# Kernel optimization log

Hardware: AMD Instinct MI355X
Metric: run time of the kernel (lower is better)

## Reference

```python
import jax, jax.numpy as jnp
import numpy as np

STATE_DIM = 16
CHANNELS = 256
LENGTH = 8192
SAMPLE_RATE = 100.0


def setup_inputs() -> dict:
    key = jax.random.key(0)
    ks = jax.random.split(key, 4)
    fan = 1.0 / np.sqrt(CHANNELS)  # lecun-normal-ish scale, flax Dense default
    x = jax.random.normal(ks[0], (LENGTH, CHANNELS), dtype=jnp.float32)
    logA = jnp.log(1.0 + jnp.arange(STATE_DIM, dtype=jnp.float32))  # module's Ainit
    W_dt = jax.random.normal(ks[1], (CHANNELS, CHANNELS), dtype=jnp.float32) * fan
    b_dt = jnp.zeros((CHANNELS,), dtype=jnp.float32)
    W_B = jax.random.normal(ks[2], (CHANNELS, STATE_DIM), dtype=jnp.float32) * fan
    b_B = jnp.zeros((STATE_DIM,), dtype=jnp.float32)
    W_C = jax.random.normal(ks[3], (CHANNELS, STATE_DIM), dtype=jnp.float32) * fan
    b_C = jnp.zeros((STATE_DIM,), dtype=jnp.float32)
    return {"x": x, "logA": logA, "W_dt": W_dt, "b_dt": b_dt,
            "W_B": W_B, "b_B": b_B, "W_C": W_C, "b_C": b_C}


def reference(x, logA, W_dt, b_dt, W_B, b_B, W_C, b_C):
    # x: (L, C)
    A = -jnp.exp(logA)                                   # (S,)
    dt = jax.nn.softplus(1.0 / SAMPLE_RATE + x @ W_dt + b_dt)  # (L, C)
    B = 1.0 + x @ W_B + b_B                              # (L, S)
    C = x @ W_C + b_C                                    # (L, S)
    # discretize: Adiscr = exp(A * dt), shape (L, C, S)
    Adiscr = jnp.exp(dt[:, :, None] * A[None, None, :])
    # Bdiscr = exp((Adiscr - 1) * (B / A))  (faithful to source, incl. outer exp)
    Bdiscr = jnp.exp((Adiscr - 1.0) * (B / A)[:, None, :])  # (L, C, S)
    u = Bdiscr * x[:, :, None]                           # (L, C, S)

    def ssm_scan(p1, p2):
        (A1, c1), (A2, c2) = p1, p2
        return (A2 * A1, c2 + A2 * c1)

    _, h = jax.lax.associative_scan(ssm_scan, (Adiscr, u))  # h: (L, C, S)
    y = jnp.einsum('ls,lcs->lc', C, h)                    # (L, C)
    return y
```

## Files before the change

### kernel.cpp

```cpp
#include <hip/hip_runtime.h>
#include <hip/hip_bf16.h>
#include <math.h>

#define LL 8192
#define CC 256
#define SS 16
#define NJ (CC*SS)
#define GG 512
#define TT 16
#define SEGS 16
#define PER (GG/SEGS)

#define LOG2E 1.4426950408889634f
#define LN2   0.6931471805599453f

typedef __attribute__((ext_vector_type(8))) short short8;
typedef __attribute__((ext_vector_type(4))) float floatx4;

__device__ __forceinline__ float fexp2(float v){ return __builtin_amdgcn_exp2f(v); }
__device__ __forceinline__ float flog2v(float v){ return __builtin_amdgcn_logf(v); }

__device__ __forceinline__ float softplus(float z){
    float t = fexp2(-fabsf(z) * LOG2E);
    return fmaxf(z, 0.f) + LN2 * flog2v(1.f + t);
}

__device__ __forceinline__ void load16(float* d, const float* __restrict__ p){
    *(float4*)&d[0]  = *(const float4*)&p[0];
    *(float4*)&d[4]  = *(const float4*)&p[4];
    *(float4*)&d[8]  = *(const float4*)&p[8];
    *(float4*)&d[12] = *(const float4*)&p[12];
}

__device__ __forceinline__ unsigned short f2b(float f){
    __hip_bfloat16 h = __float2bfloat16(f);
    return *(unsigned short*)&h;
}
__device__ __forceinline__ float b2f(unsigned short u){
    __hip_bfloat16 h = *(__hip_bfloat16*)&u;
    return __bfloat162float(h);
}

#define MBM 64
#define MBN 32
#define MBK 64
#define ASTR 72

__global__ __launch_bounds__(256,4) void k_mm(
    const float* __restrict__ x,
    const float* __restrict__ Wdt, const float* __restrict__ WB,
    const float* __restrict__ WC,
    const float* __restrict__ bdt, const float* __restrict__ bB,
    const float* __restrict__ bC, const float* __restrict__ logA,
    float* __restrict__ dt, float* __restrict__ boa, float* __restrict__ cm)
{
    __shared__ unsigned short Ah[MBM*ASTR];
    __shared__ unsigned short Al[MBM*ASTR];
    __shared__ unsigned short Bh[MBN*ASTR];
    __shared__ unsigned short Bl[MBN*ASTR];

    const int tid  = threadIdx.x;
    const int row0 = blockIdx.x * MBM;
    const int n0   = blockIdx.y * MBN;

    const int lane = tid & 63;
    const int wv   = tid >> 6;
    const int wm   = wv >> 1;
    const int wn   = wv & 1;
    const int m16  = lane & 15;
    const int q    = lane >> 4;

    const int bn  = tid & 31;
    const int bkb = (tid >> 5) * 8;
    const int bcol = n0 + bn;
    const float* __restrict__ wp;
    int wstride;
    if (bcol < 256)      { wp = Wdt + bcol;       wstride = CC; }
    else if (bcol < 272) { wp = WB  + (bcol-256); wstride = SS; }
    else                 { wp = WC  + (bcol-272); wstride = SS; }

    floatx4 acc[2];
    acc[0] = (floatx4){0.f,0.f,0.f,0.f};
    acc[1] = (floatx4){0.f,0.f,0.f,0.f};

    for (int k0 = 0; k0 < CC; k0 += MBK) {
        __syncthreads();
        #pragma unroll
        for (int h2 = 0; h2 < 2; h2++){
            int chunk = tid + h2*256;
            int r    = chunk >> 3;
            int koff = (chunk & 7) * 8;
            float4 f0 = *(const float4*)&x[(size_t)(row0+r)*CC + k0 + koff];
            float4 f1 = *(const float4*)&x[(size_t)(row0+r)*CC + k0 + koff + 4];
            float fv[8] = {f0.x,f0.y,f0.z,f0.w,f1.x,f1.y,f1.z,f1.w};
            unsigned short hs[8], ls[8];
            #pragma unroll
            for (int i=0;i<8;i++){
                hs[i] = f2b(fv[i]);
                ls[i] = f2b(fv[i] - b2f(hs[i]));
            }
            uint4 ph, pl;
            ph.x = (unsigned)hs[0] | ((unsigned)hs[1] << 16);
            ph.y = (unsigned)hs[2] | ((unsigned)hs[3] << 16);
            ph.z = (unsigned)hs[4] | ((unsigned)hs[5] << 16);
            ph.w = (unsigned)hs[6] | ((unsigned)hs[7] << 16);
            pl.x = (unsigned)ls[0] | ((unsigned)ls[1] << 16);
            pl.y = (unsigned)ls[2] | ((unsigned)ls[3] << 16);
            pl.z = (unsigned)ls[4] | ((unsigned)ls[5] << 16);
            pl.w = (unsigned)ls[6] | ((unsigned)ls[7] << 16);
            *(uint4*)&Ah[r*ASTR + koff] = ph;
            *(uint4*)&Al[r*ASTR + koff] = pl;
        }
        {
            unsigned short hs[8], ls[8];
            #pragma unroll
            for (int i=0;i<8;i++){
                float v = wp[(size_t)(k0 + bkb + i)*wstride];
                hs[i] = f2b(v);
                ls[i] = f2b(v - b2f(hs[i]));
            }
            uint4 ph, pl;
            ph.x = (unsigned)hs[0] | ((unsigned)hs[1] << 16);
            ph.y = (unsigned)hs[2] | ((unsigned)hs[3] << 16);
            ph.z = (unsigned)hs[4] | ((unsigned)hs[5] << 16);
            ph.w = (unsigned)hs[6] | ((unsigned)hs[7] << 16);
            pl.x = (unsigned)ls[0] | ((unsigned)ls[1] << 16);
            pl.y = (unsigned)ls[2] | ((unsigned)ls[3] << 16);
            pl.z = (unsigned)ls[4] | ((unsigned)ls[5] << 16);
            pl.w = (unsigned)ls[6] | ((unsigned)ls[7] << 16);
            *(uint4*)&Bh[bn*ASTR + bkb] = ph;
            *(uint4*)&Bl[bn*ASTR + bkb] = pl;
        }
        __syncthreads();

        #pragma unroll
        for (int ks = 0; ks < MBK; ks += 32) {
            short8 bh = *(const short8*)&Bh[(wn*16 + m16)*ASTR + ks + q*8];
            short8 bl = *(const short8*)&Bl[(wn*16 + m16)*ASTR + ks + q*8];
            #pragma unroll
            for (int mt = 0; mt < 2; mt++){
                short8 ah = *(const short8*)&Ah[(wm*32 + mt*16 + m16)*ASTR + ks + q*8];
                short8 al = *(const short8*)&Al[(wm*32 + mt*16 + m16)*ASTR + ks + q*8];
                acc[mt] = __builtin_amdgcn_mfma_f32_16x16x32_bf16(al, bh, acc[mt], 0, 0, 0);
                acc[mt] = __builtin_amdgcn_mfma_f32_16x16x32_bf16(ah, bl, acc[mt], 0, 0, 0);
                acc[mt] = __builtin_amdgcn_mfma_f32_16x16x32_bf16(ah, bh, acc[mt], 0, 0, 0);
            }
        }
    }

    const int col = n0 + wn*16 + m16;
    if (col < 256) {
        float bias = bdt[col];
        #pragma unroll
        for (int mt = 0; mt < 2; mt++){
            #pragma unroll
            for (int r = 0; r < 4; r++){
                int row = row0 + wm*32 + mt*16 + q*4 + r;
                dt[(size_t)row*CC + col] = softplus(0.01f + acc[mt][r] + bias);
            }
        }
    } else if (col < 272) {
        int s = col - 256;
        float A = -fexp2(logA[s] * LOG2E);
        float sc = LOG2E / A;
        float bias = bB[s];
        #pragma unroll
        for (int mt = 0; mt < 2; mt++){
            #pragma unroll
            for (int r = 0; r < 4; r++){
                int row = row0 + wm*32 + mt*16 + q*4 + r;
                boa[(size_t)row*SS + s] = (1.f + acc[mt][r] + bias) * sc;
            }
        }
    } else {
        int s = col - 272;
        float bias = bC[s];
        #pragma unroll
        for (int mt = 0; mt < 2; mt++){
            #pragma unroll
            for (int r = 0; r < 4; r++){
                int row = row0 + wm*32 + mt*16 + q*4 + r;
                cm[(size_t)row*SS + s] = acc[mt][r] + bias;
            }
        }
    }
}

__global__ __launch_bounds__(256) void k_scan1(const float* __restrict__ dt,
    const float* __restrict__ x, const float* __restrict__ boa,
    const float* __restrict__ logA,
    float* __restrict__ Ap, float* __restrict__ Hl)
{
    const int c = threadIdx.x;
    const int g = blockIdx.x;
    const int row0 = g * TT;

    __shared__ float boS[TT*SS];
    boS[c] = boa[(size_t)row0*SS + c];

    float Al2[SS];
    #pragma unroll
    for (int s=0;s<SS;s++) Al2[s] = -fexp2(logA[s]*LOG2E) * LOG2E;

    const float* __restrict__ dp = dt + (size_t)row0*CC + c;
    const float* __restrict__ xp = x  + (size_t)row0*CC + c;

    float Apr[SS], h[SS];
    #pragma unroll
    for (int s=0;s<SS;s++){ Apr[s]=1.f; h[s]=0.f; }

    __syncthreads();

    #pragma unroll
    for (int t=0;t<TT;t++){
        float d  = dp[t*CC];
        float xv = xp[t*CC];
        float bo[SS]; load16(bo, &boS[t*SS]);
        #pragma unroll
        for (int s=0;s<SS;s++){
            float a = fexp2(d * Al2[s]);
            float u = fexp2(fmaf(a, bo[s], -bo[s])) * xv;
            h[s] = fmaf(a, h[s], u);
            Apr[s] *= a;
        }
    }

    const size_t base = (size_t)g*NJ + c*SS;
    *(float4*)&Ap[base+0]  = make_float4(Apr[0],Apr[1],Apr[2],Apr[3]);
    *(float4*)&Ap[base+4]  = make_float4(Apr[4],Apr[5],Apr[6],Apr[7]);
    *(float4*)&Ap[base+8]  = make_float4(Apr[8],Apr[9],Apr[10],Apr[11]);
    *(float4*)&Ap[base+12] = make_float4(Apr[12],Apr[13],Apr[14],Apr[15]);
    *(float4*)&Hl[base+0]  = make_float4(h[0],h[1],h[2],h[3]);
    *(float4*)&Hl[base+4]  = make_float4(h[4],h[5],h[6],h[7]);
    *(float4*)&Hl[base+8]  = make_float4(h[8],h[9],h[10],h[11]);
    *(float4*)&Hl[base+12] = make_float4(h[12],h[13],h[14],h[15]);
}

__global__ __launch_bounds__(256) void k_carry(const float* __restrict__ Ap,
    const float* __restrict__ Hl, float* __restrict__ Cr)
{
    const int tid = threadIdx.x;
    const int jl  = tid & 15;
    const int seg = tid >> 4;
    const int j   = blockIdx.x * 16 + jl;

    const size_t base = (size_t)(seg*PER)*NJ + j;

    float a[PER], u[PER];
    #pragma unroll
    for (int k=0;k<PER;k++){
        a[k] = Ap[base + (size_t)k*NJ];
        u[k] = Hl[base + (size_t)k*NJ];
    }
    float Aag = 1.f, Uag = 0.f;
    #pragma unroll
    for (int k=0;k<PER;k++){ Uag = fmaf(a[k], Uag, u[k]); Aag *= a[k]; }

    __shared__ float As[SEGS][17], Us[SEGS][17];
    As[seg][jl] = Aag; Us[seg][jl] = Uag;
    __syncthreads();
    float hin = 0.f;
    for (int t = 0; t < seg; ++t)
        hin = fmaf(As[t][jl], hin, Us[t][jl]);

    float h = hin;
    #pragma unroll
    for (int k=0;k<PER;k++){
        Cr[base + (size_t)k*NJ] = h;
        h = fmaf(a[k], h, u[k]);
    }
}

__global__ __launch_bounds__(256) void k_scan2(const float* __restrict__ dt,
    const float* __restrict__ x, const float* __restrict__ boa,
    const float* __restrict__ cmat, const float* __restrict__ logA,
    const float* __restrict__ Cr, float* __restrict__ y)
{
    const int c = threadIdx.x;
    const int g = blockIdx.x;
    const int row0 = g * TT;

    __shared__ float boS[TT*SS], cmS[TT*SS];
    boS[c] = boa [(size_t)row0*SS + c];
    cmS[c] = cmat[(size_t)row0*SS + c];

    float Al2[SS];
    #pragma unroll
    for (int s=0;s<SS;s++) Al2[s] = -fexp2(logA[s]*LOG2E) * LOG2E;

    const float* __restrict__ dp = dt + (size_t)row0*CC + c;
    const float* __restrict__ xp = x  + (size_t)row0*CC + c;
    float* __restrict__ yp = y + (size_t)row0*CC + c;

    float h[SS];
    load16(h, &Cr[(size_t)g*NJ + c*SS]);

    __syncthreads();

    #pragma unroll
    for (int t=0;t<TT;t++){
        float d  = dp[t*CC];
        float xv = xp[t*CC];
        float bo[SS]; load16(bo, &boS[t*SS]);
        float cmv[SS]; load16(cmv, &cmS[t*SS]);
        float yv = 0.f;
        #pragma unroll
        for (int s=0;s<SS;s++){
            float a = fexp2(d * Al2[s]);
            float u = fexp2(fmaf(a, bo[s], -bo[s])) * xv;
            h[s] = fmaf(a, h[s], u);
            yv = fmaf(cmv[s], h[s], yv);
        }
        yp[t*CC] = yv;
    }
}

extern "C" void kernel_launch(void* const* d_in, const int* in_sizes, int n_in,
                              void* d_out, int out_size, void* d_ws, size_t ws_size,
                              hipStream_t stream) {
    const float* x    = (const float*)d_in[0];
    const float* logA = (const float*)d_in[1];
    const float* W_dt = (const float*)d_in[2];
    const float* b_dt = (const float*)d_in[3];
    const float* W_B  = (const float*)d_in[4];
    const float* b_B  = (const float*)d_in[5];
    const float* W_C  = (const float*)d_in[6];
    const float* b_C  = (const float*)d_in[7];
    float* y  = (float*)d_out;
    float* ws = (float*)d_ws;

    float* dt   = ws;
    float* boa  = dt   + (size_t)LL*CC;
    float* cmv  = boa  + (size_t)LL*SS;
    float* Ap   = cmv  + (size_t)LL*SS;
    float* Hl   = Ap   + (size_t)GG*NJ;
    float* Cr   = Hl   + (size_t)GG*NJ;

    hipLaunchKernelGGL(k_mm,   dim3(128,9), dim3(256), 0, stream,
                       x, W_dt, W_B, W_C, b_dt, b_B, b_C, logA, dt, boa, cmv);
    hipLaunchKernelGGL(k_scan1, dim3(GG), dim3(256), 0, stream,
                       dt, x, boa, logA, Ap, Hl);
    hipLaunchKernelGGL(k_carry, dim3(NJ/16), dim3(256), 0, stream, Ap, Hl, Cr);
    hipLaunchKernelGGL(k_scan2, dim3(GG), dim3(256), 0, stream,
                       dt, x, boa, cmv, logA, Cr, y);
}
```

Baseline: 122.3 us.

## Split state dimension across four lanes per channel and lengthen scan chunks

The two chunked-scan kernels now give each thread one channel and 4 of the 16 state components, with a 2D grid (chunks × channel blocks). y is combined across the four lanes with xor shuffles. Chunk length doubles to 32 rows and the chunk count halves to 256, which also halves the Ap/Hl/Cr carry traffic and the k_carry work. The goal is to cut per-thread register pressure and increase thread-level parallelism and occupancy. The cost is redundant dt/x loads across the four lanes, a longer serial chain per thread, and shuffle overhead.

```diff
diff --git a/kernel.cpp b/kernel.cpp
--- a/kernel.cpp
+++ b/kernel.cpp
@@ -6,8 +6,10 @@
 #define CC 256
 #define SS 16
 #define NJ (CC*SS)
-#define GG 512
-#define TT 16
+#define GG 256
+#define TT 32
+#define SP 4
+#define CB 64
 #define SEGS 16
 #define PER (GG/SEGS)
 
@@ -23,13 +25,6 @@
 __device__ __forceinline__ float softplus(float z){
     float t = fexp2(-fabsf(z) * LOG2E);
     return fmaxf(z, 0.f) + LN2 * flog2v(1.f + t);
-}
-
-__device__ __forceinline__ void load16(float* d, const float* __restrict__ p){
-    *(float4*)&d[0]  = *(const float4*)&p[0];
-    *(float4*)&d[4]  = *(const float4*)&p[4];
-    *(float4*)&d[8]  = *(const float4*)&p[8];
-    *(float4*)&d[12] = *(const float4*)&p[12];
 }
 
 __device__ __forceinline__ unsigned short f2b(float f){
@@ -191,49 +186,43 @@
     const float* __restrict__ logA,
     float* __restrict__ Ap, float* __restrict__ Hl)
 {
-    const int c = threadIdx.x;
-    const int g = blockIdx.x;
+    const int tid = threadIdx.x;
+    const int sg  = tid & 3;
+    const int cl  = tid >> 2;
+    const int g   = blockIdx.x;
+    const int c   = blockIdx.y * CB + cl;
     const int row0 = g * TT;
 
-    __shared__ float boS[TT*SS];
-    boS[c] = boa[(size_t)row0*SS + c];
-
-    float Al2[SS];
-    #pragma unroll
-    for (int s=0;s<SS;s++) Al2[s] = -fexp2(logA[s]*LOG2E) * LOG2E;
-
-    const float* __restrict__ dp = dt + (size_t)row0*CC + c;
-    const float* __restrict__ xp = x  + (size_t)row0*CC + c;
-
-    float Apr[SS], h[SS];
-    #pragma unroll
-    for (int s=0;s<SS;s++){ Apr[s]=1.f; h[s]=0.f; }
-
-    __syncthreads();
-
-    #pragma unroll
+    float Al2[SP];
+    #pragma unroll
+    for (int i=0;i<SP;i++) Al2[i] = -fexp2(logA[sg*SP+i]*LOG2E) * LOG2E;
+
+    const float* __restrict__ dp = dt  + (size_t)row0*CC + c;
+    const float* __restrict__ xp = x   + (size_t)row0*CC + c;
+    const float* __restrict__ bp = boa + (size_t)row0*SS + sg*SP;
+
+    float Apr[SP], h[SP];
+    #pragma unroll
+    for (int i=0;i<SP;i++){ Apr[i]=1.f; h[i]=0.f; }
+
+    #pragma unroll 8
     for (int t=0;t<TT;t++){
-        float d  = dp[t*CC];
-        float xv = xp[t*CC];
-        float bo[SS]; load16(bo, &boS[t*SS]);
-        #pragma unroll
-        for (int s=0;s<SS;s++){
+        float d  = dp[(size_t)t*CC];
+        float xv = xp[(size_t)t*CC];
+        float4 bo = *(const float4*)&bp[(size_t)t*SS];
+        float bov[SP] = {bo.x, bo.y, bo.z, bo.w};
+        #pragma unroll
+        for (int s=0;s<SP;s++){
             float a = fexp2(d * Al2[s]);
-            float u = fexp2(fmaf(a, bo[s], -bo[s])) * xv;
+            float u = fexp2(fmaf(a, bov[s], -bov[s])) * xv;
             h[s] = fmaf(a, h[s], u);
             Apr[s] *= a;
         }
     }
 
-    const size_t base = (size_t)g*NJ + c*SS;
-    *(float4*)&Ap[base+0]  = make_float4(Apr[0],Apr[1],Apr[2],Apr[3]);
-    *(float4*)&Ap[base+4]  = make_float4(Apr[4],Apr[5],Apr[6],Apr[7]);
-    *(float4*)&Ap[base+8]  = make_float4(Apr[8],Apr[9],Apr[10],Apr[11]);
-    *(float4*)&Ap[base+12] = make_float4(Apr[12],Apr[13],Apr[14],Apr[15]);
-    *(float4*)&Hl[base+0]  = make_float4(h[0],h[1],h[2],h[3]);
-    *(float4*)&Hl[base+4]  = make_float4(h[4],h[5],h[6],h[7]);
-    *(float4*)&Hl[base+8]  = make_float4(h[8],h[9],h[10],h[11]);
-    *(float4*)&Hl[base+12] = make_float4(h[12],h[13],h[14],h[15]);
+    const size_t base = (size_t)g*NJ + (size_t)c*SS + sg*SP;
+    *(float4*)&Ap[base] = make_float4(Apr[0],Apr[1],Apr[2],Apr[3]);
+    *(float4*)&Hl[base] = make_float4(h[0],h[1],h[2],h[3]);
 }
 
 __global__ __launch_bounds__(256) void k_carry(const float* __restrict__ Ap,
@@ -276,42 +265,48 @@
     const float* __restrict__ cmat, const float* __restrict__ logA,
     const float* __restrict__ Cr, float* __restrict__ y)
 {
-    const int c = threadIdx.x;
-    const int g = blockIdx.x;
+    const int tid = threadIdx.x;
+    const int sg  = tid & 3;
+    const int cl  = tid >> 2;
+    const int g   = blockIdx.x;
+    const int c   = blockIdx.y * CB + cl;
     const int row0 = g * TT;
 
-    __shared__ float boS[TT*SS], cmS[TT*SS];
-    boS[c] = boa [(size_t)row0*SS + c];
-    cmS[c] = cmat[(size_t)row0*SS + c];
-
-    float Al2[SS];
-    #pragma unroll
-    for (int s=0;s<SS;s++) Al2[s] = -fexp2(logA[s]*LOG2E) * LOG2E;
-
-    const float* __restrict__ dp = dt + (size_t)row0*CC + c;
-    const float* __restrict__ xp = x  + (size_t)row0*CC + c;
+    float Al2[SP];
+    #pragma unroll
+    for (int i=0;i<SP;i++) Al2[i] = -fexp2(logA[sg*SP+i]*LOG2E) * LOG2E;
+
+    const float* __restrict__ dp = dt   + (size_t)row0*CC + c;
+    const float* __restrict__ xp = x    + (size_t)row0*CC + c;
+    const float* __restrict__ bp = boa  + (size_t)row0*SS + sg*SP;
+    const float* __restrict__ cp = cmat + (size_t)row0*SS + sg*SP;
     float* __restrict__ yp = y + (size_t)row0*CC + c;
 
-    float h[SS];
-    load16(h, &Cr[(size_t)g*NJ + c*SS]);
-
-    __syncthreads();
-
-    #pragma unroll
+    float h[SP];
+    {
+        float4 hc = *(const float4*)&Cr[(size_t)g*NJ + (size_t)c*SS + sg*SP];
+        h[0]=hc.x; h[1]=hc.y; h[2]=hc.z; h[3]=hc.w;
+    }
+
+    #pragma unroll 8
     for (int t=0;t<TT;t++){
-        float d  = dp[t*CC];
-        float xv = xp[t*CC];
-        float bo[SS]; load16(bo, &boS[t*SS]);
-        float cmv[SS]; load16(cmv, &cmS[t*SS]);
+        float d  = dp[(size_t)t*CC];
+        float xv = xp[(size_t)t*CC];
+        float4 bo = *(const float4*)&bp[(size_t)t*SS];
+        float4 cv = *(const float4*)&cp[(size_t)t*SS];
+        float bov[SP] = {bo.x,bo.y,bo.z,bo.w};
+        float cvv[SP] = {cv.x,cv.y,cv.z,cv.w};
         float yv = 0.f;
         #pragma unroll
-        for (int s=0;s<SS;s++){
+        for (int s=0;s<SP;s++){
             float a = fexp2(d * Al2[s]);
-            float u = fexp2(fmaf(a, bo[s], -bo[s])) * xv;
+            float u = fexp2(fmaf(a, bov[s], -bov[s])) * xv;
             h[s] = fmaf(a, h[s], u);
-            yv = fmaf(cmv[s], h[s], yv);
-        }
-        yp[t*CC] = yv;
+            yv = fmaf(cvv[s], h[s], yv);
+        }
+        yv += __shfl_xor(yv, 1);
+        yv += __shfl_xor(yv, 2);
+        if (sg == 0) yp[(size_t)t*CC] = yv;
     }
 }
 
@@ -338,9 +333,9 @@
 
     hipLaunchKernelGGL(k_mm,   dim3(128,9), dim3(256), 0, stream,
                        x, W_dt, W_B, W_C, b_dt, b_B, b_C, logA, dt, boa, cmv);
-    hipLaunchKernelGGL(k_scan1, dim3(GG), dim3(256), 0, stream,
+    hipLaunchKernelGGL(k_scan1, dim3(GG,4), dim3(256), 0, stream,
                        dt, x, boa, logA, Ap, Hl);
     hipLaunchKernelGGL(k_carry, dim3(NJ/16), dim3(256), 0, stream, Ap, Hl, Cr);
-    hipLaunchKernelGGL(k_scan2, dim3(GG), dim3(256), 0, stream,
+    hipLaunchKernelGGL(k_scan2, dim3(GG,4), dim3(256), 0, stream,
                        dt, x, boa, cmv, logA, Cr, y);
 }
```

Result: no change. 121.7 us (-0.4%).
